# Kernel optimization log

Measured on AMD Instinct MI355X. Metric: run time of the kernel, lower is better.

Reference implementation:

```python
import jax, jax.numpy as jnp
import numpy as np

CELL = 50.0  # cubic box edge length (self.cell)
N_ATOMS = 100000
N_PAIRS = 6400000
N_TABLE = 1024
EPS = 1e-12


def setup_inputs() -> dict:
    key = jax.random.key(0)
    k1, k2, k3 = jax.random.split(key, 3)
    # positions inside the box
    q = jax.random.uniform(k1, (N_ATOMS, 3), dtype=jnp.float32) * CELL
    # neighbor pair list [E,2] (each pair listed once; forces scattered to both ends)
    nbr_list = jax.random.randint(k2, (N_PAIRS, 2), 0, N_ATOMS, dtype=jnp.int32)
    # tabulated force: r grid (sorted, covers max minimum-image distance) and force values
    r_max = CELL * np.sqrt(3.0) / 2.0
    table_r = jnp.linspace(0.1, r_max, N_TABLE, dtype=jnp.float32)
    table_f = jax.random.normal(k3, (N_TABLE,), dtype=jnp.float32)
    return {"q": q, "nbr_list": nbr_list, "table_r": table_r, "table_f": table_f}


def reference(q, nbr_list, table_r, table_f):
    i = nbr_list[:, 0]
    j = nbr_list[:, 1]
    # pair displacement with minimum-image convention in a cubic cell
    d = q[i] - q[j]                                  # [E,3]
    d = d - CELL * jnp.round(d / CELL)
    pdist = jnp.sqrt(jnp.sum(d * d, axis=-1, keepdims=True))  # [E,1]
    unit_vector = d / jnp.maximum(pdist, EPS)        # [E,3]
    # tabulated force magnitude lookup (GPU-side interpolation replacing scipy interp1d)
    force_magnitude = jnp.interp(pdist[:, 0], table_r, table_f)[:, None]  # [E,1]
    force_vector = force_magnitude * unit_vector     # [E,3]
    # scatter-add to atoms (index_add_ on dim 0, + on i, - on j)
    force = jnp.zeros_like(q).at[i].add(force_vector).at[j].add(-force_vector)
    return force
```

## Files before the change

### kernel.cpp

```cpp
#include <hip/hip_runtime.h>

#define CELL 50.0f
#define N_TABLE 1024
#define NB 1024
#define NBLK 512
#define THREADS 256
#define SCAT_THREADS 512
#define LBUF_CAP 25088
#define RED_THREADS 512
#define PHASE_CAP 9216

typedef unsigned int uint;
typedef unsigned long long ull;

__global__ __launch_bounds__(THREADS) void pack_q4_kernel(
    const float* __restrict__ q, float4* __restrict__ q4, int n_atoms)
{
    int i = blockIdx.x * THREADS + threadIdx.x;
    if (i < n_atoms)
        q4[i] = make_float4(q[3 * i], q[3 * i + 1], q[3 * i + 2], 0.0f);
}

__global__ __launch_bounds__(THREADS) void hist_kernel(
    const int2* __restrict__ nbr, uint* __restrict__ partial,
    uint* __restrict__ rawh, int n_pairs, int ppb)
{
    __shared__ uint h[NB];
    for (int k = threadIdx.x; k < NB; k += THREADS) h[k] = 0;
    __syncthreads();
    int start = blockIdx.x * ppb;
    int end   = min(start + ppb, n_pairs & ~1);
    const int4* nbr4 = (const int4*)nbr;
    for (int p2 = (start >> 1) + threadIdx.x; p2 < (end >> 1); p2 += THREADS) {
        int4 v = nbr4[p2];
        atomicAdd(&h[((uint)v.x) >> 7], 1u);
        atomicAdd(&h[((uint)v.y) >> 7], 1u);
        atomicAdd(&h[((uint)v.z) >> 7], 1u);
        atomicAdd(&h[((uint)v.w) >> 7], 1u);
    }
    if (blockIdx.x == 0 && threadIdx.x == 0 && (n_pairs & 1)) {
        int2 ij = nbr[n_pairs - 1];
        atomicAdd(&h[((uint)ij.x) >> 7], 1u);
        atomicAdd(&h[((uint)ij.y) >> 7], 1u);
    }
    __syncthreads();
    for (int k = threadIdx.x; k < NB; k += THREADS) {
        uint c = h[k];
        partial[k * NBLK + blockIdx.x] = c;
        rawh[blockIdx.x * NB + k]      = c;
    }
}

__global__ __launch_bounds__(THREADS) void scan_rows_kernel(
    uint* __restrict__ partial, uint* __restrict__ binTotal)
{
    __shared__ uint s[THREADS];
    int bin = blockIdx.x;
    uint running = 0;
    for (int c = 0; c < NBLK / THREADS; c++) {
        int idx = bin * NBLK + c * THREADS + threadIdx.x;
        uint v = partial[idx];
        s[threadIdx.x] = v;
        __syncthreads();
        for (int off = 1; off < THREADS; off <<= 1) {
            uint t = (threadIdx.x >= (uint)off) ? s[threadIdx.x - off] : 0u;
            __syncthreads();
            s[threadIdx.x] += t;
            __syncthreads();
        }
        partial[idx] = running + s[threadIdx.x] - v;
        uint csum = s[THREADS - 1];
        __syncthreads();
        running += csum;
    }
    if (threadIdx.x == 0) binTotal[bin] = running;
}

__global__ __launch_bounds__(THREADS) void scan_totals_kernel(
    const uint* __restrict__ binTotal, uint* __restrict__ binBase)
{
    __shared__ uint s[THREADS];
    uint v[4];
    uint sum = 0;
    int base = threadIdx.x * 4;
    for (int k = 0; k < 4; k++) { v[k] = binTotal[base + k]; sum += v[k]; }
    s[threadIdx.x] = sum;
    __syncthreads();
    for (int off = 1; off < THREADS; off <<= 1) {
        uint t = (threadIdx.x >= (uint)off) ? s[threadIdx.x - off] : 0u;
        __syncthreads();
        s[threadIdx.x] += t;
        __syncthreads();
    }
    uint run = s[threadIdx.x] - sum;
    for (int k = 0; k < 4; k++) { binBase[base + k] = run; run += v[k]; }
    if (threadIdx.x == THREADS - 1) binBase[NB] = run;
}

__global__ __launch_bounds__(SCAT_THREADS) void scatter_sorted_kernel(
    const int2* __restrict__ nbr, const uint* __restrict__ rawh,
    const uint* __restrict__ partial, const uint* __restrict__ binBase,
    uint* __restrict__ entries, int n_pairs, int ppb)
{
    __shared__ uint lbuf[LBUF_CAP];
    __shared__ uint localBase[NB];
    __shared__ uint lcur[NB];
    __shared__ uint gcur[NB];
    __shared__ uint ssc[SCAT_THREADS];

    int tid = threadIdx.x;
    int blk = blockIdx.x;

    for (int k = tid; k < NB; k += SCAT_THREADS)
        gcur[k] = binBase[k] + partial[k * NBLK + blk];

    uint v0 = rawh[blk * NB + 2 * tid];
    uint v1 = rawh[blk * NB + 2 * tid + 1];
    uint sum2 = v0 + v1;
    ssc[tid] = sum2;
    __syncthreads();
    for (int off = 1; off < SCAT_THREADS; off <<= 1) {
        uint t = (tid >= off) ? ssc[tid - off] : 0u;
        __syncthreads();
        ssc[tid] += t;
        __syncthreads();
    }
    uint base = ssc[tid] - sum2;
    localBase[2 * tid]     = base;      lcur[2 * tid]     = base;
    localBase[2 * tid + 1] = base + v0; lcur[2 * tid + 1] = base + v0;
    __syncthreads();

    int start = blk * ppb;
    int end   = min(start + ppb, n_pairs & ~1);
    const int4* nbr4 = (const int4*)nbr;
    int lim = end >> 1;
    int p2  = (start >> 1) + tid;
    if (p2 < lim) {
        int4 v = nbr4[p2];
        for (;;) {
            int pn = p2 + SCAT_THREADS;
            int4 vnext;
            bool has = pn < lim;
            if (has) vnext = nbr4[pn];
            uint i0 = (uint)v.x, j0 = (uint)v.y, i1 = (uint)v.z, j1 = (uint)v.w;
            uint o0 = atomicAdd(&lcur[i0 >> 7], 1u);
            uint o1 = atomicAdd(&lcur[j0 >> 7], 1u);
            uint o2 = atomicAdd(&lcur[i1 >> 7], 1u);
            uint o3 = atomicAdd(&lcur[j1 >> 7], 1u);
            lbuf[o0] = (j0 << 7) | (i0 & 127u);
            lbuf[o1] = (i0 << 7) | (j0 & 127u);
            lbuf[o2] = (j1 << 7) | (i1 & 127u);
            lbuf[o3] = (i1 << 7) | (j1 & 127u);
            if (!has) break;
            v = vnext; p2 = pn;
        }
    }
    if (blk == 0 && tid == 0 && (n_pairs & 1)) {
        int2 ij = nbr[n_pairs - 1];
        uint i = (uint)ij.x, j = (uint)ij.y;
        uint o;
        o = atomicAdd(&lcur[i >> 7], 1u); lbuf[o] = (j << 7) | (i & 127u);
        o = atomicAdd(&lcur[j >> 7], 1u); lbuf[o] = (i << 7) | (j & 127u);
    }
    __syncthreads();

    int wave = tid >> 6, lane = tid & 63;
    for (int b = wave; b < NB; b += SCAT_THREADS / 64) {
        uint lb  = localBase[b];
        uint cnt = lcur[b] - lb;
        if (!cnt) continue;
        uint gdst = gcur[b];
        for (uint o = lane; o < cnt; o += 64)
            entries[gdst + o] = lbuf[lb + o];
    }
}

__global__ __launch_bounds__(THREADS) void scatter_plain_kernel(
    const int2* __restrict__ nbr, const uint* __restrict__ partial,
    const uint* __restrict__ binBase, uint* __restrict__ entries,
    int n_pairs, int ppb)
{
    __shared__ uint cur[NB];
    for (int k = threadIdx.x; k < NB; k += THREADS)
        cur[k] = binBase[k] + partial[k * NBLK + blockIdx.x];
    __syncthreads();
    int start = blockIdx.x * ppb;
    int end   = min(start + ppb, n_pairs & ~1);
    const int4* nbr4 = (const int4*)nbr;
    for (int p2 = (start >> 1) + threadIdx.x; p2 < (end >> 1); p2 += THREADS) {
        int4 v = nbr4[p2];
        uint i0 = (uint)v.x, j0 = (uint)v.y, i1 = (uint)v.z, j1 = (uint)v.w;
        uint p;
        p = atomicAdd(&cur[i0 >> 7], 1u); entries[p] = (j0 << 7) | (i0 & 127u);
        p = atomicAdd(&cur[j0 >> 7], 1u); entries[p] = (i0 << 7) | (j0 & 127u);
        p = atomicAdd(&cur[i1 >> 7], 1u); entries[p] = (j1 << 7) | (i1 & 127u);
        p = atomicAdd(&cur[j1 >> 7], 1u); entries[p] = (i1 << 7) | (j1 & 127u);
    }
    if (blockIdx.x == 0 && threadIdx.x == 0 && (n_pairs & 1)) {
        int2 ij = nbr[n_pairs - 1];
        uint i = (uint)ij.x, j = (uint)ij.y;
        uint p;
        p = atomicAdd(&cur[i >> 7], 1u); entries[p] = (j << 7) | (i & 127u);
        p = atomicAdd(&cur[j >> 7], 1u); entries[p] = (i << 7) | (j & 127u);
    }
}

__device__ __forceinline__ void phys_acc(
    float ax, float ay, float az, float ox, float oy, float oz,
    const float* __restrict__ tfa, const float* __restrict__ tfd,
    float r0, float inv_dr, float& fx, float& fy, float& fz)
{
    float dx = ax - ox, dy = ay - oy, dz = az - oz;
    dx -= (dx > 25.0f) ? 50.0f : ((dx < -25.0f) ? -50.0f : 0.0f);
    dy -= (dy > 25.0f) ? 50.0f : ((dy < -25.0f) ? -50.0f : 0.0f);
    dz -= (dz > 25.0f) ? 50.0f : ((dz < -25.0f) ? -50.0f : 0.0f);
    float r2 = dx * dx + dy * dy + dz * dz;
    float rs = __builtin_amdgcn_rsqf(fmaxf(r2, 1e-24f));
    float r  = r2 * rs;
    float t  = (r - r0) * inv_dr;
    t = fminf(fmaxf(t, 0.0f), 1023.0f);
    int idx = min((int)t, N_TABLE - 2);
    float frac = t - (float)idx;
    float sm = (tfa[idx] + frac * tfd[idx]) * rs;
    fx += sm * dx; fy += sm * dy; fz += sm * dz;
}

template<int USE_Q4>
__global__ __launch_bounds__(RED_THREADS) void reduce_sorted_kernel(
    const float* __restrict__ q, const float4* __restrict__ q4,
    const float* __restrict__ table_r, const float* __restrict__ table_f,
    const uint* __restrict__ binBase, const uint* __restrict__ entries,
    float* __restrict__ force, int n_atoms)
{
    __shared__ float tfa[N_TABLE];
    __shared__ float tfd[N_TABLE];
    __shared__ uint  sorted[PHASE_CAP];
    __shared__ uint  hcnt[128], hcur[128], hstart[128], sscan[128];
    __shared__ float paccx[RED_THREADS], paccy[RED_THREADS], paccz[RED_THREADS];

    int b = blockIdx.x, tid = threadIdx.x;
    int atomBase = b << 7;
    if (atomBase >= n_atoms) return;
    int nA = min(128, n_atoms - atomBase);

    const float r0     = table_r[0];
    const float rend   = table_r[N_TABLE - 1];
    const float inv_dr = (float)(N_TABLE - 1) / (rend - r0);

    for (int k = tid; k < N_TABLE - 1; k += RED_THREADS) {
        float a = table_f[k];
        tfa[k] = a; tfd[k] = table_f[k + 1] - a;
    }
    paccx[tid] = 0.0f; paccy[tid] = 0.0f; paccz[tid] = 0.0f;

    int a = tid & 127, s4 = tid >> 7;
    float ax = 0.0f, ay = 0.0f, az = 0.0f;
    if (a < nA) {
        if (USE_Q4) { float4 v = q4[atomBase + a]; ax = v.x; ay = v.y; az = v.z; }
        else {
            ax = q[(atomBase + a) * 3];
            ay = q[(atomBase + a) * 3 + 1];
            az = q[(atomBase + a) * 3 + 2];
        }
    }

    uint e0 = binBase[b], e1 = binBase[b + 1];

    for (uint es = e0; es < e1; es += PHASE_CAP) {
        uint ee = min(es + PHASE_CAP, e1);

        if (tid < 128) hcnt[tid] = 0;
        __syncthreads();

        for (uint e = es + tid; e < ee; e += RED_THREADS)
            atomicAdd(&hcnt[entries[e] & 127u], 1u);
        __syncthreads();

        if (tid < 128) sscan[tid] = hcnt[tid];
        __syncthreads();
        for (int off = 1; off < 128; off <<= 1) {
            uint t = 0;
            if (tid < 128 && tid >= off) t = sscan[tid - off];
            __syncthreads();
            if (tid < 128) sscan[tid] += t;
            __syncthreads();
        }
        if (tid < 128) {
            uint s0 = sscan[tid] - hcnt[tid];
            hstart[tid] = s0; hcur[tid] = s0;
        }
        __syncthreads();

        for (uint e = es + tid; e < ee; e += RED_THREADS) {
            uint ev = entries[e];
            uint p  = atomicAdd(&hcur[ev & 127u], 1u);
            sorted[p] = ev >> 7;
        }
        __syncthreads();

        {
            uint st  = hstart[a];
            uint cnt = hcnt[a];
            uint chunk = (cnt + 3) >> 2;
            uint k0 = min((uint)s4 * chunk, cnt);
            uint k1 = min(k0 + chunk, cnt);
            float fx = 0.0f, fy = 0.0f, fz = 0.0f;

            uint k = k0;
            for (; k + 4 <= k1; k += 4) {
                uint o0 = sorted[st + k],     o1 = sorted[st + k + 1];
                uint o2 = sorted[st + k + 2], o3 = sorted[st + k + 3];
                float x0, y0, z0, x1, y1, z1, x2, y2, z2, x3, y3, z3;
                if (USE_Q4) {
                    float4 g0 = q4[o0], g1 = q4[o1], g2 = q4[o2], g3 = q4[o3];
                    x0 = g0.x; y0 = g0.y; z0 = g0.z;
                    x1 = g1.x; y1 = g1.y; z1 = g1.z;
                    x2 = g2.x; y2 = g2.y; z2 = g2.z;
                    x3 = g3.x; y3 = g3.y; z3 = g3.z;
                } else {
                    x0 = q[3*o0]; y0 = q[3*o0+1]; z0 = q[3*o0+2];
                    x1 = q[3*o1]; y1 = q[3*o1+1]; z1 = q[3*o1+2];
                    x2 = q[3*o2]; y2 = q[3*o2+1]; z2 = q[3*o2+2];
                    x3 = q[3*o3]; y3 = q[3*o3+1]; z3 = q[3*o3+2];
                }
                phys_acc(ax, ay, az, x0, y0, z0, tfa, tfd, r0, inv_dr, fx, fy, fz);
                phys_acc(ax, ay, az, x1, y1, z1, tfa, tfd, r0, inv_dr, fx, fy, fz);
                phys_acc(ax, ay, az, x2, y2, z2, tfa, tfd, r0, inv_dr, fx, fy, fz);
                phys_acc(ax, ay, az, x3, y3, z3, tfa, tfd, r0, inv_dr, fx, fy, fz);
            }
            for (; k < k1; ++k) {
                uint o = sorted[st + k];
                float ox, oy, oz;
                if (USE_Q4) { float4 g = q4[o]; ox = g.x; oy = g.y; oz = g.z; }
                else { ox = q[3*o]; oy = q[3*o+1]; oz = q[3*o+2]; }
                phys_acc(ax, ay, az, ox, oy, oz, tfa, tfd, r0, inv_dr, fx, fy, fz);
            }
            paccx[tid] += fx; paccy[tid] += fy; paccz[tid] += fz;
        }
        __syncthreads();
    }

    for (int k = tid; k < nA; k += RED_THREADS) {
        float sx = paccx[k] + paccx[k + 128] + paccx[k + 256] + paccx[k + 384];
        float sy = paccy[k] + paccy[k + 128] + paccy[k + 256] + paccy[k + 384];
        float sz = paccz[k] + paccz[k + 128] + paccz[k + 256] + paccz[k + 384];
        force[(atomBase + k) * 3 + 0] = sx;
        force[(atomBase + k) * 3 + 1] = sy;
        force[(atomBase + k) * 3 + 2] = sz;
    }
}

__global__ __launch_bounds__(THREADS) void pair_force_atomic_kernel(
    const float* __restrict__ q, const int2* __restrict__ nbr,
    const float* __restrict__ table_r, const float* __restrict__ table_f,
    float* __restrict__ force, int n_pairs)
{
    __shared__ float tr[N_TABLE];
    __shared__ float tf[N_TABLE];
    for (int k = threadIdx.x; k < N_TABLE; k += THREADS) { tr[k] = table_r[k]; tf[k] = table_f[k]; }
    __syncthreads();
    const float r0 = tr[0], rend = tr[N_TABLE - 1];
    const float inv_dr = (float)(N_TABLE - 1) / (rend - r0);
    int p = blockIdx.x * THREADS + threadIdx.x;
    if (p >= n_pairs) return;
    int2 ij = nbr[p];
    int i = ij.x, j = ij.y;
    float dx = q[3 * i] - q[3 * j], dy = q[3 * i + 1] - q[3 * j + 1], dz = q[3 * i + 2] - q[3 * j + 2];
    dx -= CELL * rintf(dx / CELL); dy -= CELL * rintf(dy / CELL); dz -= CELL * rintf(dz / CELL);
    float r = sqrtf(dx * dx + dy * dy + dz * dz);
    float inv = 1.0f / fmaxf(r, 1e-12f);
    float fm;
    if (r <= r0) fm = tf[0];
    else if (r >= rend) fm = tf[N_TABLE - 1];
    else {
        float t = (r - r0) * inv_dr;
        int idx = min(max((int)t, 0), N_TABLE - 2);
        if (r < tr[idx]) idx = max(idx - 1, 0);
        else if (r >= tr[idx + 1]) idx = min(idx + 1, N_TABLE - 2);
        float rl = tr[idx], rh = tr[idx + 1];
        fm = tf[idx] + (r - rl) * (tf[idx + 1] - tf[idx]) / (rh - rl);
    }
    float s = fm * inv;
    float fx = s * dx, fy = s * dy, fz = s * dz;
    atomicAdd(&force[3 * i + 0], fx); atomicAdd(&force[3 * i + 1], fy); atomicAdd(&force[3 * i + 2], fz);
    atomicAdd(&force[3 * j + 0], -fx); atomicAdd(&force[3 * j + 1], -fy); atomicAdd(&force[3 * j + 2], -fz);
}

extern "C" void kernel_launch(void* const* d_in, const int* in_sizes, int n_in,
                              void* d_out, int out_size, void* d_ws, size_t ws_size,
                              hipStream_t stream) {
    const float* q       = (const float*)d_in[0];
    const int2*  nbr     = (const int2*)d_in[1];
    const float* table_r = (const float*)d_in[2];
    const float* table_f = (const float*)d_in[3];
    float*       force   = (float*)d_out;

    const int n_pairs = in_sizes[1] / 2;
    const int n_atoms = in_sizes[0] / 3;

    size_t off_partial  = 0;
    size_t off_rawh     = (off_partial + (size_t)NB * NBLK * 4 + 255) & ~255ull;
    size_t off_binTotal = (off_rawh + (size_t)NB * NBLK * 4 + 255) & ~255ull;
    size_t off_binBase  = (off_binTotal + (size_t)NB * 4 + 255) & ~255ull;
    size_t off_entries  = (off_binBase + (size_t)(NB + 1) * 4 + 255) & ~255ull;
    size_t off_q4       = (off_entries + (size_t)2 * n_pairs * 4 + 255) & ~255ull;
    size_t need_base    = off_q4;
    size_t need_q4      = off_q4 + (size_t)n_atoms * 16;

    if (ws_size < need_base || n_atoms > NB * 128) {
        hipMemsetAsync(d_out, 0, (size_t)out_size * sizeof(float), stream);
        int blocks = (n_pairs + THREADS - 1) / THREADS;
        pair_force_atomic_kernel<<<blocks, THREADS, 0, stream>>>(q, nbr, table_r, table_f, force, n_pairs);
        return;
    }

    char* ws = (char*)d_ws;
    uint*   partial  = (uint*)(ws + off_partial);
    uint*   rawh     = (uint*)(ws + off_rawh);
    uint*   binTotal = (uint*)(ws + off_binTotal);
    uint*   binBase  = (uint*)(ws + off_binBase);
    uint*   entries  = (uint*)(ws + off_entries);
    float4* q4       = (float4*)(ws + off_q4);
    int use_q4 = (ws_size >= need_q4) ? 1 : 0;

    int ppb = (((n_pairs + NBLK - 1) / NBLK) + 1) & ~1;

    if (use_q4) {
        int pb = (n_atoms + THREADS - 1) / THREADS;
        pack_q4_kernel<<<pb, THREADS, 0, stream>>>(q, q4, n_atoms);
    }
    hist_kernel<<<NBLK, THREADS, 0, stream>>>(nbr, partial, rawh, n_pairs, ppb);
    scan_rows_kernel<<<NB, THREADS, 0, stream>>>(partial, binTotal);
    scan_totals_kernel<<<1, THREADS, 0, stream>>>(binTotal, binBase);
    if (2 * ppb <= LBUF_CAP)
        scatter_sorted_kernel<<<NBLK, SCAT_THREADS, 0, stream>>>(
            nbr, rawh, partial, binBase, entries, n_pairs, ppb);
    else
        scatter_plain_kernel<<<NBLK, THREADS, 0, stream>>>(
            nbr, partial, binBase, entries, n_pairs, ppb);
    if (use_q4)
        reduce_sorted_kernel<1><<<NB, RED_THREADS, 0, stream>>>(q, q4, table_r, table_f, binBase, entries, force, n_atoms);
    else
        reduce_sorted_kernel<0><<<NB, RED_THREADS, 0, stream>>>(q, q4, table_r, table_f, binBase, entries, force, n_atoms);
}
```

Baseline: 183.6 us.

## Balance sorted-entry reduction by splitting segments evenly across threads with run-length flush

Replaces the per-atom work split (each atom's entries split across four threads) with an even split of all sorted entries in a phase across the 512 threads. Each thread walks its contiguous slice, detects changes of local atom id, and flushes partial sums to shared accumulators with shared-memory atomics. Own-atom positions are staged in shared memory, and the gathers are batched six at a time for more memory-level parallelism. This removes the load imbalance caused by uneven per-atom neighbor counts, at the cost of shared atomics and a data-dependent branch per entry.

```diff
diff --git a/kernel.cpp b/kernel.cpp
--- a/kernel.cpp
+++ b/kernel.cpp
@@ -235,8 +235,9 @@
     __shared__ float tfa[N_TABLE];
     __shared__ float tfd[N_TABLE];
     __shared__ uint  sorted[PHASE_CAP];
-    __shared__ uint  hcnt[128], hcur[128], hstart[128], sscan[128];
-    __shared__ float paccx[RED_THREADS], paccy[RED_THREADS], paccz[RED_THREADS];
+    __shared__ uint  hcnt[128], hcur[128], sscan[128];
+    __shared__ float qsx[128], qsy[128], qsz[128];
+    __shared__ float paccx[128], paccy[128], paccz[128];
 
     int b = blockIdx.x, tid = threadIdx.x;
     int atomBase = b << 7;
@@ -251,23 +252,23 @@
         float a = table_f[k];
         tfa[k] = a; tfd[k] = table_f[k + 1] - a;
     }
-    paccx[tid] = 0.0f; paccy[tid] = 0.0f; paccz[tid] = 0.0f;
-
-    int a = tid & 127, s4 = tid >> 7;
-    float ax = 0.0f, ay = 0.0f, az = 0.0f;
-    if (a < nA) {
-        if (USE_Q4) { float4 v = q4[atomBase + a]; ax = v.x; ay = v.y; az = v.z; }
-        else {
-            ax = q[(atomBase + a) * 3];
-            ay = q[(atomBase + a) * 3 + 1];
-            az = q[(atomBase + a) * 3 + 2];
-        }
+    if (tid < 128) {
+        paccx[tid] = 0.0f; paccy[tid] = 0.0f; paccz[tid] = 0.0f;
+        if (tid < nA) {
+            if (USE_Q4) { float4 v = q4[atomBase + tid]; qsx[tid] = v.x; qsy[tid] = v.y; qsz[tid] = v.z; }
+            else {
+                qsx[tid] = q[(atomBase + tid) * 3];
+                qsy[tid] = q[(atomBase + tid) * 3 + 1];
+                qsz[tid] = q[(atomBase + tid) * 3 + 2];
+            }
+        } else { qsx[tid] = 0.0f; qsy[tid] = 0.0f; qsz[tid] = 0.0f; }
     }
 
     uint e0 = binBase[b], e1 = binBase[b + 1];
 
     for (uint es = e0; es < e1; es += PHASE_CAP) {
-        uint ee = min(es + PHASE_CAP, e1);
+        uint ee  = min(es + PHASE_CAP, e1);
+        uint cnt = ee - es;
 
         if (tid < 128) hcnt[tid] = 0;
         __syncthreads();
@@ -285,68 +286,69 @@
             if (tid < 128) sscan[tid] += t;
             __syncthreads();
         }
-        if (tid < 128) {
-            uint s0 = sscan[tid] - hcnt[tid];
-            hstart[tid] = s0; hcur[tid] = s0;
-        }
+        if (tid < 128) hcur[tid] = sscan[tid] - hcnt[tid];
         __syncthreads();
 
         for (uint e = es + tid; e < ee; e += RED_THREADS) {
             uint ev = entries[e];
             uint p  = atomicAdd(&hcur[ev & 127u], 1u);
-            sorted[p] = ev >> 7;
+            sorted[p] = ev;
         }
         __syncthreads();
 
         {
-            uint st  = hstart[a];
-            uint cnt = hcnt[a];
-            uint chunk = (cnt + 3) >> 2;
-            uint k0 = min((uint)s4 * chunk, cnt);
-            uint k1 = min(k0 + chunk, cnt);
+            uint seg = (cnt + RED_THREADS - 1) / RED_THREADS;
+            uint k0 = min((uint)tid * seg, cnt);
+            uint k1 = min(k0 + seg, cnt);
+            int curL = -1;
             float fx = 0.0f, fy = 0.0f, fz = 0.0f;
-
-            uint k = k0;
-            for (; k + 4 <= k1; k += 4) {
-                uint o0 = sorted[st + k],     o1 = sorted[st + k + 1];
-                uint o2 = sorted[st + k + 2], o3 = sorted[st + k + 3];
-                float x0, y0, z0, x1, y1, z1, x2, y2, z2, x3, y3, z3;
-                if (USE_Q4) {
-                    float4 g0 = q4[o0], g1 = q4[o1], g2 = q4[o2], g3 = q4[o3];
-                    x0 = g0.x; y0 = g0.y; z0 = g0.z;
-                    x1 = g1.x; y1 = g1.y; z1 = g1.z;
-                    x2 = g2.x; y2 = g2.y; z2 = g2.z;
-                    x3 = g3.x; y3 = g3.y; z3 = g3.z;
-                } else {
-                    x0 = q[3*o0]; y0 = q[3*o0+1]; z0 = q[3*o0+2];
-                    x1 = q[3*o1]; y1 = q[3*o1+1]; z1 = q[3*o1+2];
-                    x2 = q[3*o2]; y2 = q[3*o2+1]; z2 = q[3*o2+2];
-                    x3 = q[3*o3]; y3 = q[3*o3+1]; z3 = q[3*o3+2];
+            float sx = 0.0f, sy = 0.0f, sz = 0.0f;
+
+            for (uint k = k0; k < k1; k += 6) {
+                uint n = min(6u, k1 - k);
+                uint ev[6];
+                float gx[6], gy[6], gz[6];
+                #pragma unroll
+                for (uint t = 0; t < 6; t++)
+                    ev[t] = sorted[k + (t < n ? t : 0u)];
+                #pragma unroll
+                for (uint t = 0; t < 6; t++) {
+                    uint o = ev[t] >> 7;
+                    if (USE_Q4) { float4 g = q4[o]; gx[t] = g.x; gy[t] = g.y; gz[t] = g.z; }
+                    else { gx[t] = q[3 * o]; gy[t] = q[3 * o + 1]; gz[t] = q[3 * o + 2]; }
                 }
-                phys_acc(ax, ay, az, x0, y0, z0, tfa, tfd, r0, inv_dr, fx, fy, fz);
-                phys_acc(ax, ay, az, x1, y1, z1, tfa, tfd, r0, inv_dr, fx, fy, fz);
-                phys_acc(ax, ay, az, x2, y2, z2, tfa, tfd, r0, inv_dr, fx, fy, fz);
-                phys_acc(ax, ay, az, x3, y3, z3, tfa, tfd, r0, inv_dr, fx, fy, fz);
+                #pragma unroll
+                for (uint t = 0; t < 6; t++) {
+                    if (t < n) {
+                        int l = (int)(ev[t] & 127u);
+                        if (l != curL) {
+                            if (curL >= 0) {
+                                atomicAdd(&paccx[curL], fx);
+                                atomicAdd(&paccy[curL], fy);
+                                atomicAdd(&paccz[curL], fz);
+                            }
+                            curL = l;
+                            sx = qsx[l]; sy = qsy[l]; sz = qsz[l];
+                            fx = 0.0f; fy = 0.0f; fz = 0.0f;
+                        }
+                        phys_acc(sx, sy, sz, gx[t], gy[t], gz[t], tfa, tfd, r0, inv_dr, fx, fy, fz);
+                    }
+                }
             }
-            for (; k < k1; ++k) {
-                uint o = sorted[st + k];
-                float ox, oy, oz;
-                if (USE_Q4) { float4 g = q4[o]; ox = g.x; oy = g.y; oz = g.z; }
-                else { ox = q[3*o]; oy = q[3*o+1]; oz = q[3*o+2]; }
-                phys_acc(ax, ay, az, ox, oy, oz, tfa, tfd, r0, inv_dr, fx, fy, fz);
+            if (curL >= 0) {
+                atomicAdd(&paccx[curL], fx);
+                atomicAdd(&paccy[curL], fy);
+                atomicAdd(&paccz[curL], fz);
             }
-            paccx[tid] += fx; paccy[tid] += fy; paccz[tid] += fz;
         }
         __syncthreads();
     }
 
+    __syncthreads();
     for (int k = tid; k < nA; k += RED_THREADS) {
-        float sx = paccx[k] + paccx[k + 128] + paccx[k + 256] + paccx[k + 384];
-        float sy = paccy[k] + paccy[k + 128] + paccy[k + 256] + paccy[k + 384];
-        float sz = paccz[k] + paccz[k + 128] + paccz[k + 256] + paccz[k + 384];
-        force[(atomBase + k) * 3 + 0] = sx;
-        force[(atomBase + k) * 3 + 1] = sy;
-        force[(atomBase + k) * 3 + 2] = sz;
+        force[(atomBase + k) * 3 + 0] = paccx[k];
+        force[(atomBase + k) * 3 + 1] = paccy[k];
+        force[(atomBase + k) * 3 + 2] = paccz[k];
     }
 }
 
```

Result: slower. 193.7 us (+5.5%).
